# Kernel tuning notes

Hardware: AMD Instinct MI355X
Metric: run time of the kernel (lower is better)

The kernel has to match this reference:

```python
import jax, jax.numpy as jnp
import numpy as np

B, C, T, NB, NF = 4, 256, 128, 64, 512

def _rms(x, w, eps=1e-6):
    # RMSNorm over channel dim (axis=1) of NCHW tensor
    return x * jax.lax.rsqrt(jnp.mean(x * x, axis=1, keepdims=True) + eps) * w[None, :, None, None]

def _conv1(x, w, b):
    # 1x1 conv: w is [out, in]
    return jnp.einsum('bchw,oc->bohw', x, w) + b[None, :, None, None]

def _swiglu(x, iw, ib, ow, ob):
    h = _conv1(x, iw, ib)
    a, g = jnp.split(h, 2, axis=1)
    return _conv1(a * jax.nn.silu(g), ow, ob)

def setup_inputs() -> dict:
    key = jax.random.key(0)
    ks = iter(jax.random.split(key, 32))
    s = lambda shape, scale: jax.random.normal(next(ks), shape, jnp.float32) * scale
    wsc = 1.0 / np.sqrt(C)
    return {
        'latent': s((B, C, T, NB), 1.0),
        'side': s((B, C, T, NF), 1.0),
        'expansion_basis': s((1, NB, 1, NF), 1.0),
        'lp_norm_w': jnp.ones((C,), jnp.float32),
        'lp_w': s((C, C), wsc), 'lp_b': jnp.zeros((C,), jnp.float32),
        'qn_w': jnp.ones((C,), jnp.float32),
        'qmlp_in_w': s((2 * C, C), wsc), 'qmlp_in_b': jnp.zeros((2 * C,), jnp.float32),
        'qmlp_out_w': s((C, C), wsc), 'qmlp_out_b': jnp.zeros((C,), jnp.float32),
        'q_w': s((C, C), wsc), 'q_b': jnp.zeros((C,), jnp.float32),
        'k_w': s((C, C), wsc), 'k_b': jnp.zeros((C,), jnp.float32),
        'v_w': s((C, C), wsc), 'v_b': jnp.zeros((C,), jnp.float32),
        'o_w': s((C, C), wsc), 'o_b': jnp.zeros((C,), jnp.float32),
        'ffn_norm_w': jnp.ones((C,), jnp.float32),
        'ffn_in_w': s((2 * C, C), wsc), 'ffn_in_b': jnp.zeros((2 * C,), jnp.float32),
        'ffn_out_w': s((C, C), wsc), 'ffn_out_b': jnp.zeros((C,), jnp.float32),
        'score_scale': jnp.asarray(1.0 / np.sqrt(C), jnp.float32),
        'prior_scale': jnp.asarray(1.0, jnp.float32),
        'query_skip_scale': jnp.asarray(1.0, jnp.float32),
    }

def reference(latent, side, expansion_basis, lp_norm_w, lp_w, lp_b, qn_w,
              qmlp_in_w, qmlp_in_b, qmlp_out_w, qmlp_out_b,
              q_w, q_b, k_w, k_b, v_w, v_b, o_w, o_b,
              ffn_norm_w, ffn_in_w, ffn_in_b, ffn_out_w, ffn_out_b,
              score_scale, prior_scale, query_skip_scale):
    # latent_pre: RMSNorm -> 1x1 conv -> SiLU
    latent_h = jax.nn.silu(_conv1(_rms(latent, lp_norm_w), lp_w, lp_b))  # [B,C,T,NB]
    # adaptive query path
    query_h = _swiglu(_rms(side, qn_w), qmlp_in_w, qmlp_in_b, qmlp_out_w, qmlp_out_b)  # [B,C,T,NF]
    q = _conv1(query_h, q_w, q_b)   # [B,C,T,NF]
    k = _conv1(latent_h, k_w, k_b)  # [B,C,T,NB]
    v = _conv1(latent_h, v_w, v_b)  # [B,C,T,NB]
    # scores: [B,T,NF,NB], contraction over channel
    scores = jnp.einsum('bctf,bctn->btfn', q, k) * score_scale
    bias = expansion_basis[0, :, 0, :].T  # [NF, NB]
    scores = scores + bias[None, None] * prior_scale
    weights = jax.nn.softmax(scores, axis=-1)
    attended = jnp.einsum('btfn,bctn->bctf', weights, v)  # [B,C,T,NF]
    hidden = _conv1(attended, o_w, o_b) + query_h * query_skip_scale
    hidden = hidden + _swiglu(_rms(hidden, ffn_norm_w), ffn_in_w, ffn_in_b, ffn_out_w, ffn_out_b)
    return hidden
```

## Files before the change

kernel.cpp:

```cpp
#include <hip/hip_runtime.h>
#include <stdint.h>
#include <stddef.h>

#define B_ 4
#define C_ 256
#define T_ 128
#define NB_ 64
#define NF_ 512
#define PLAT_ (T_*NB_)
#define PSIDE_ (T_*NF_)

using bf16x8 = __attribute__((ext_vector_type(8))) short;
using bf16x4 = __attribute__((ext_vector_type(4))) short;
using f32x4  = __attribute__((ext_vector_type(4))) float;

__device__ __forceinline__ float b2f(unsigned short h) {
  unsigned int u = ((unsigned int)h) << 16;
  return __builtin_bit_cast(float, u);
}
__device__ __forceinline__ float b2f(short h) {
  unsigned int u = ((unsigned int)(unsigned short)h) << 16;
  return __builtin_bit_cast(float, u);
}
__device__ __forceinline__ unsigned short f2b(float f) {
  unsigned int u = __builtin_bit_cast(unsigned int, f);
  u += 0x7FFFu + ((u >> 16) & 1u);
  return (unsigned short)(u >> 16);
}

__device__ __forceinline__ bf16x8 ld8(const unsigned short* p) {
  return *(const bf16x8*)p;
}
__device__ __forceinline__ bf16x8 ld8(const float* p) {
  float4 a = *(const float4*)p;
  float4 b = *(const float4*)(p + 4);
  bf16x8 r;
  r[0] = (short)f2b(a.x); r[1] = (short)f2b(a.y);
  r[2] = (short)f2b(a.z); r[3] = (short)f2b(a.w);
  r[4] = (short)f2b(b.x); r[5] = (short)f2b(b.y);
  r[6] = (short)f2b(b.z); r[7] = (short)f2b(b.w);
  return r;
}
__device__ __forceinline__ void stv(float* p, float v) { *p = v; }
__device__ __forceinline__ void stv(unsigned short* p, float v) { *p = f2b(v); }

__device__ __forceinline__ void gload16(const void* g, void* l) {
  __builtin_amdgcn_global_load_lds(
      (const __attribute__((address_space(1))) void*)g,
      (__attribute__((address_space(3))) void*)l, 16, 0, 0);
}

__device__ __forceinline__ int u4i(int r) { return (r ^ (r >> 2)) & 3; }

enum { EPI_NONE = 0, EPI_SILU = 1, EPI_RESID = 3, EPI_SWIGLU = 4, EPI_DUALX = 5 };

__global__ __launch_bounds__(256) void wprep_k(const float* __restrict__ w,
                                               const float* __restrict__ nw,
                                               unsigned short* __restrict__ out, int n)
{
  int i = blockIdx.x * 256 + threadIdx.x;
  if (i < n) out[i] = f2b(w[i] * nw[i & 255]);
}

__global__ __launch_bounds__(256) void cvt_k(const float* __restrict__ in,
                                             unsigned short* __restrict__ out, int n)
{
  int i = blockIdx.x * 256 + threadIdx.x;
  if (i < n) out[i] = f2b(in[i]);
}

__global__ __launch_bounds__(256) void wscale_k(const float* __restrict__ w,
                                                const float* __restrict__ s,
                                                unsigned short* __restrict__ out, int n)
{
  int i = blockIdx.x * 256 + threadIdx.x;
  if (i < n) out[i] = f2b(w[i] * s[0]);
}

__global__ __launch_bounds__(256) void foldw_k(const float* __restrict__ A,
                                               const float* __restrict__ Bm,
                                               unsigned short* __restrict__ out)
{
  const int m = blockIdx.x;
  const int c = threadIdx.x;
  float acc = 0.f;
  #pragma unroll 8
  for (int j = 0; j < C_; ++j) acc = fmaf(A[m * C_ + j], Bm[j * C_ + c], acc);
  out[m * C_ + c] = f2b(acc);
}

__global__ __launch_bounds__(256) void foldb_k(const float* __restrict__ A,
                                               const float* __restrict__ bin,
                                               const float* __restrict__ badd,
                                               float* __restrict__ bout)
{
  const int m = threadIdx.x;
  float acc = 0.f;
  #pragma unroll 8
  for (int j = 0; j < C_; ++j) acc = fmaf(A[m * C_ + j], bin[j], acc);
  bout[m] = acc + badd[m];
}

__global__ __launch_bounds__(256) void bcomb_k(const float* __restrict__ b0,
                                               const float* __restrict__ b1,
                                               const float* __restrict__ s,
                                               float* __restrict__ bout)
{
  const int m = threadIdx.x;
  bout[m] = b0[m] + s[0] * b1[m];
}

template<int EPI, bool RMS, bool XT, typename TY, bool YT, int CFG, bool CSIN>
__global__ __launch_bounds__(256, 2) void gemm_k(
    const void* __restrict__ Xv,
    const void* __restrict__ Xv2,
    const unsigned short* __restrict__ W,
    const float* __restrict__ bias,
    TY* Y,
    const unsigned short* __restrict__ RT,
    float* pscale,
    int Xs, int Xoff, int Ys, int Yoff, int Ps)
{
  constexpr bool WDUAL = (EPI == EPI_SWIGLU) || (EPI == EPI_DUALX);
  constexpr bool GDUAL = (EPI == EPI_SWIGLU);
  constexpr bool XDUAL = (EPI == EPI_DUALX);
  constexpr int BM  = (CFG == 0) ? 256 : 128;
  constexpr int NWV = (CFG == 0) ? 1 : 2;
  constexpr int WN  = 64 / NWV;
  constexpr int NFR = WN / 16;
  constexpr int RW  = (WDUAL ? 2 : 1) * BM;
  constexpr int XR  = (XDUAL ? 2 : 1) * 64;

  __shared__ unsigned short sA[RW * 32];
  __shared__ unsigned short sX[XR * 32];
  __shared__ float red[4][64];

  const int tid = threadIdx.x;
  const int lane = tid & 63;
  const int wid = tid >> 6;
  const int l15 = lane & 15;
  const int q4 = lane >> 4;
  const int z = blockIdx.z;
  const int p0 = ((CFG == 0) ? blockIdx.x : (blockIdx.x >> 1)) * 64;
  const int m0 = (CFG == 0) ? 0 : (blockIdx.x & 1) * BM;
  const int mh = (CFG == 0) ? wid : (wid >> 1);
  const int nh = (CFG == 0) ? 0 : (wid & 1);

  const float* Xf = nullptr;
  const unsigned short* Xt = nullptr;
  const unsigned short* Xt2 = nullptr;
  if constexpr (XT) {
    Xt = (const unsigned short*)Xv + ((size_t)z * Xs + Xoff + p0) * C_;
    if constexpr (XDUAL)
      Xt2 = (const unsigned short*)Xv2 + ((size_t)z * Xs + Xoff + p0) * C_;
  } else {
    Xf = (const float*)Xv + (size_t)z * C_ * Xs + Xoff + p0;
  }

  const f32x4 zf = {0.f, 0.f, 0.f, 0.f};
  f32x4 acc0[4][NFR];
  f32x4 acc1[GDUAL ? 4 : 1][NFR];
  #pragma unroll
  for (int i = 0; i < 4; ++i)
    #pragma unroll
    for (int j = 0; j < NFR; ++j) {
      acc0[i][j] = zf;
      if constexpr (GDUAL) acc1[i][j] = zf;
    }

  float sq = 0.f;

  for (int kt = 0; kt < 8; ++kt) {
    if constexpr (XT) {
      const int row = wid * 16 + (lane >> 2);
      const int chunk = (lane & 3) ^ u4i(row);
      const size_t soff = (size_t)row * C_ + kt * 32 + (chunk << 3);
      gload16(Xt + soff, &sX[(wid * 16) * 32]);
      if constexpr (XDUAL) gload16(Xt2 + soff, &sX[(64 + wid * 16) * 32]);
    } else {
      const float* xp = Xf + (size_t)(kt * 32 + wid * 8) * Xs + lane;
      float v[8];
      #pragma unroll
      for (int j = 0; j < 8; ++j) v[j] = xp[(size_t)j * Xs];
      bf16x8 w8;
      #pragma unroll
      for (int j = 0; j < 8; ++j) {
        if constexpr (RMS) sq = fmaf(v[j], v[j], sq);
        w8[j] = (short)f2b(v[j]);
      }
      *(bf16x8*)((char*)sX + lane * 64 + ((wid ^ u4i(lane)) << 4)) = w8;
    }
    #pragma unroll
    for (int it = 0; it < RW / 64; ++it) {
      const int rbase = wid * (RW / 4) + it * 16;
      const int rl = rbase + (lane >> 2);
      const int bank = rl / BM;
      const int rloc = rl & (BM - 1);
      const int chunk = (lane & 3) ^ u4i(rl);
      gload16(W + (size_t)(bank * C_ + m0 + rloc) * C_ + kt * 32 + (chunk << 3),
              &sA[rbase * 32]);
    }
    __syncthreads();

    bf16x8 af0[4], af1[4], bfr[NFR], bfr2[NFR];
    #pragma unroll
    for (int mf = 0; mf < 4; ++mf) {
      const int r = mh * 64 + mf * 16 + l15;
      const int sl = (q4 ^ u4i(r)) << 3;
      af0[mf] = *(const bf16x8*)(&sA[r * 32 + sl]);
      if constexpr (WDUAL) af1[mf] = *(const bf16x8*)(&sA[(BM + r) * 32 + sl]);
    }
    #pragma unroll
    for (int nf = 0; nf < NFR; ++nf) {
      const int n = nh * WN + nf * 16 + l15;
      const int sl = (q4 ^ u4i(n)) << 3;
      bfr[nf] = *(const bf16x8*)(&sX[n * 32 + sl]);
      if constexpr (XDUAL) bfr2[nf] = *(const bf16x8*)(&sX[(64 + n) * 32 + sl]);
    }
    #pragma unroll
    for (int mf = 0; mf < 4; ++mf)
      #pragma unroll
      for (int nf = 0; nf < NFR; ++nf) {
        acc0[mf][nf] = __builtin_amdgcn_mfma_f32_16x16x32_bf16(af0[mf], bfr[nf], acc0[mf][nf], 0, 0, 0);
        if constexpr (GDUAL)
          acc1[mf][nf] = __builtin_amdgcn_mfma_f32_16x16x32_bf16(af1[mf], bfr[nf], acc1[mf][nf], 0, 0, 0);
        if constexpr (XDUAL)
          acc0[mf][nf] = __builtin_amdgcn_mfma_f32_16x16x32_bf16(af1[mf], bfr2[nf], acc0[mf][nf], 0, 0, 0);
      }
    __syncthreads();
  }

  float cs[NFR];
  #pragma unroll
  for (int nf = 0; nf < NFR; ++nf) cs[nf] = 1.f;
  if constexpr (RMS) {
    red[wid][lane] = sq;
    __syncthreads();
    #pragma unroll
    for (int nf = 0; nf < NFR; ++nf) {
      const int n = nh * WN + nf * 16 + l15;
      cs[nf] = rsqrtf((red[0][n] + red[1][n] + red[2][n] + red[3][n]) * (1.0f / (float)C_) + 1e-6f);
    }
  }
  if constexpr (CSIN) {
    #pragma unroll
    for (int nf = 0; nf < NFR; ++nf)
      cs[nf] = pscale[(size_t)z * Ps + p0 + nh * WN + nf * 16 + l15];
  }

  TY* Yb = nullptr;
  if constexpr (!YT) Yb = Y + (size_t)z * C_ * Ys + Yoff;

  float p2[NFR];
  #pragma unroll
  for (int nf = 0; nf < NFR; ++nf) p2[nf] = 0.f;

  #pragma unroll
  for (int mf = 0; mf < 4; ++mf) {
    const int mb = m0 + mh * 64 + mf * 16 + q4 * 4;
    const float4 b1 = *(const float4*)(bias + mb);
    float4 b2 = {0.f, 0.f, 0.f, 0.f};
    if constexpr (GDUAL) b2 = *(const float4*)(bias + C_ + mb);
    #pragma unroll
    for (int nf = 0; nf < NFR; ++nf) {
      const int pl = p0 + nh * WN + nf * 16 + l15;
      bf16x4 h4 = {0, 0, 0, 0};
      if constexpr (EPI == EPI_RESID)
        h4 = *(const bf16x4*)(RT + ((size_t)z * Ps + pl) * C_ + mb);
      if constexpr (YT) {
        bf16x4 pk;
        #pragma unroll
        for (int r = 0; r < 4; ++r) {
          float y = acc0[mf][nf][r] * cs[nf] + ((const float*)&b1)[r];
          if constexpr (EPI == EPI_SILU) y = y / (1.0f + __expf(-y));
          if constexpr (EPI == EPI_SWIGLU) {
            float g = acc1[mf][nf][r] * cs[nf] + ((const float*)&b2)[r];
            y = y * (g / (1.0f + __expf(-g)));
          }
          if constexpr (EPI == EPI_DUALX) p2[nf] = fmaf(y, y, p2[nf]);
          pk[r] = (short)f2b(y);
        }
        *(bf16x4*)(Y + ((size_t)z * Ys + Yoff + pl) * C_ + mb) = pk;
      } else {
        #pragma unroll
        for (int r = 0; r < 4; ++r) {
          const size_t oidx = (size_t)(mb + r) * Ys + pl;
          float y = acc0[mf][nf][r] * cs[nf] + ((const float*)&b1)[r];
          if constexpr (EPI == EPI_SILU) y = y / (1.0f + __expf(-y));
          if constexpr (EPI == EPI_SWIGLU) {
            float g = acc1[mf][nf][r] * cs[nf] + ((const float*)&b2)[r];
            y = y * (g / (1.0f + __expf(-g)));
          }
          if constexpr (EPI == EPI_RESID) y += b2f(h4[r]);
          stv(&Yb[oidx], y);
        }
      }
    }
  }

  if constexpr (EPI == EPI_DUALX) {
    #pragma unroll
    for (int nf = 0; nf < NFR; ++nf) {
      p2[nf] += __shfl_xor(p2[nf], 16);
      p2[nf] += __shfl_xor(p2[nf], 32);
    }
    if (q4 == 0) {
      #pragma unroll
      for (int nf = 0; nf < NFR; ++nf) red[wid][nf * 16 + l15] = p2[nf];
    }
    __syncthreads();
    if (wid == 0 && q4 == 0) {
      #pragma unroll
      for (int nf = 0; nf < NFR; ++nf) {
        const int n = nf * 16 + l15;
        const float c2 = rsqrtf((red[0][n] + red[1][n] + red[2][n] + red[3][n]) * (1.0f / (float)C_) + 1e-6f);
        pscale[(size_t)z * Ps + p0 + n] = c2;
      }
    }
  }
}

__global__ __launch_bounds__(256) void attn_k(
    const unsigned short* Q,
    const unsigned short* __restrict__ Kp,
    const unsigned short* __restrict__ Vp,
    const float* __restrict__ basis,
    const float* __restrict__ ssp,
    const float* __restrict__ psp,
    unsigned short* O,
    int PsQ, int t0, int ltc)
{
  __shared__ unsigned short sK[64 * 256];
  __shared__ unsigned short sQ[64 * 256];
  __shared__ unsigned short sV[256 * 72];
  __shared__ unsigned short sW[64 * 72];
  __shared__ unsigned short sB[64 * 72];

  const int tid = threadIdx.x;
  const int lane = tid & 63;
  const int wid = tid >> 6;
  const int l15 = lane & 15;
  const int q4 = lane >> 4;
  const int z = blockIdx.x >> ltc;
  const int tl = blockIdx.x & ((1 << ltc) - 1);

  const unsigned short* Qt = Q + ((size_t)z * PsQ + (size_t)tl * NF_) * C_;
  unsigned short*       Ot = O + ((size_t)z * PsQ + (size_t)tl * NF_) * C_;
  const unsigned short* Kt = Kp + ((size_t)z * PLAT_ + (size_t)(t0 + tl) * NB_) * C_;
  const size_t vbase = (size_t)z * C_ * PLAT_ + (size_t)(t0 + tl) * NB_;

  const float ss = ssp[0];
  const float ps = psp[0];
  const f32x4 zf = {0.f, 0.f, 0.f, 0.f};

  {
    #pragma unroll
    for (int it = 0; it < 8; ++it) {
      int i = wid * 8 + it;
      int n = 2 * i + (lane >> 5);
      int sc = (lane & 31) ^ (n & 7);
      gload16(Kt + (size_t)n * C_ + (sc << 3), &sK[i * 512]);
    }
    const int c0 = tid >> 3;
    const int n0 = (tid & 7) << 3;
    #pragma unroll
    for (int pass = 0; pass < 8; ++pass) {
      int c = c0 + pass * 32;
      bf16x8 v8 = *(const bf16x8*)(Vp + vbase + (size_t)c * PLAT_ + n0);
      *(bf16x8*)(&sV[c * 72 + n0]) = v8;
    }
  }

  for (int fc = 0; fc < 8; ++fc) {
    const int f0 = fc * 64;
    #pragma unroll
    for (int it = 0; it < 8; ++it) {
      int i = wid * 8 + it;
      int n = 2 * i + (lane >> 5);
      int sc = (lane & 31) ^ (n & 7);
      gload16(Qt + (size_t)(f0 + n) * C_ + (sc << 3), &sQ[i * 512]);
    }
    {
      const int nr = tid >> 3;
      const int fl0 = (tid & 7) << 3;
      #pragma unroll
      for (int pass = 0; pass < 2; ++pass) {
        int nn = nr + pass * 32;
        bf16x8 b8 = ld8(basis + (size_t)nn * NF_ + f0 + fl0);
        *(bf16x8*)(&sB[nn * 72 + fl0]) = b8;
      }
    }
    __syncthreads();

    f32x4 sacc[4];
    #pragma unroll
    for (int nt = 0; nt < 4; ++nt) sacc[nt] = zf;
    const int frow = wid * 16 + l15;
    const int swq = l15 & 7;
    #pragma unroll
    for (int kt = 0; kt < 8; ++kt) {
      int kb = kt * 4 + q4;
      bf16x8 a8 = *(const bf16x8*)(&sQ[frow * 256 + ((kb ^ swq) << 3)]);
      #pragma unroll
      for (int nt = 0; nt < 4; ++nt) {
        bf16x8 b8 = *(const bf16x8*)(&sK[(nt * 16 + l15) * 256 + ((kb ^ swq) << 3)]);
        sacc[nt] = __builtin_amdgcn_mfma_f32_16x16x32_bf16(a8, b8, sacc[nt], 0, 0, 0);
      }
    }

    #pragma unroll
    for (int r = 0; r < 4; ++r) {
      const int fcl = wid * 16 + q4 * 4 + r;
      float v[4];
      #pragma unroll
      for (int nt = 0; nt < 4; ++nt)
        v[nt] = sacc[nt][r] * ss + b2f(sB[(nt * 16 + l15) * 72 + fcl]) * ps;
      float mx = fmaxf(fmaxf(v[0], v[1]), fmaxf(v[2], v[3]));
      #pragma unroll
      for (int d = 1; d < 16; d <<= 1) mx = fmaxf(mx, __shfl_xor(mx, d));
      float e[4], sum = 0.f;
      #pragma unroll
      for (int nt = 0; nt < 4; ++nt) { e[nt] = __expf(v[nt] - mx); sum += e[nt]; }
      #pragma unroll
      for (int d = 1; d < 16; d <<= 1) sum += __shfl_xor(sum, d);
      float inv = 1.0f / sum;
      #pragma unroll
      for (int nt = 0; nt < 4; ++nt)
        sW[fcl * 72 + nt * 16 + l15] = f2b(e[nt] * inv);
    }
    __syncthreads();

    f32x4 pacc[4][4];
    #pragma unroll
    for (int mf = 0; mf < 4; ++mf)
      #pragma unroll
      for (int nf = 0; nf < 4; ++nf) pacc[mf][nf] = zf;
    #pragma unroll
    for (int kt = 0; kt < 2; ++kt) {
      int k0 = kt * 32 + q4 * 8;
      bf16x8 a8[4], b8[4];
      #pragma unroll
      for (int mf = 0; mf < 4; ++mf)
        a8[mf] = *(const bf16x8*)(&sV[(wid * 64 + mf * 16 + l15) * 72 + k0]);
      #pragma unroll
      for (int nf = 0; nf < 4; ++nf)
        b8[nf] = *(const bf16x8*)(&sW[(nf * 16 + l15) * 72 + k0]);
      #pragma unroll
      for (int mf = 0; mf < 4; ++mf)
        #pragma unroll
        for (int nf = 0; nf < 4; ++nf)
          pacc[mf][nf] = __builtin_amdgcn_mfma_f32_16x16x32_bf16(a8[mf], b8[nf], pacc[mf][nf], 0, 0, 0);
    }
    #pragma unroll
    for (int mf = 0; mf < 4; ++mf) {
      int cb = wid * 64 + mf * 16 + q4 * 4;
      #pragma unroll
      for (int nf = 0; nf < 4; ++nf) {
        int f = f0 + nf * 16 + l15;
        bf16x4 pk;
        #pragma unroll
        for (int r = 0; r < 4; ++r) pk[r] = (short)f2b(pacc[mf][nf][r]);
        *(bf16x4*)(Ot + (size_t)f * C_ + cb) = pk;
      }
    }
    __syncthreads();
  }
}

extern "C" void kernel_launch(void* const* d_in, const int* in_sizes, int n_in,
                              void* d_out, int out_size, void* d_ws, size_t ws_size,
                              hipStream_t stream)
{
  (void)in_sizes; (void)n_in; (void)out_size;
  const float* latent     = (const float*)d_in[0];
  const float* side       = (const float*)d_in[1];
  const float* basis      = (const float*)d_in[2];
  const float* lp_norm_w  = (const float*)d_in[3];
  const float* lp_w       = (const float*)d_in[4];
  const float* lp_b       = (const float*)d_in[5];
  const float* qn_w       = (const float*)d_in[6];
  const float* qmlp_in_w  = (const float*)d_in[7];
  const float* qmlp_in_b  = (const float*)d_in[8];
  const float* qmlp_out_w = (const float*)d_in[9];
  const float* qmlp_out_b = (const float*)d_in[10];
  const float* q_w        = (const float*)d_in[11];
  const float* q_b        = (const float*)d_in[12];
  const float* k_w        = (const float*)d_in[13];
  const float* k_b        = (const float*)d_in[14];
  const float* v_w        = (const float*)d_in[15];
  const float* v_b        = (const float*)d_in[16];
  const float* o_w        = (const float*)d_in[17];
  const float* o_b        = (const float*)d_in[18];
  const float* ffn_norm_w = (const float*)d_in[19];
  const float* ffn_in_w   = (const float*)d_in[20];
  const float* ffn_in_b   = (const float*)d_in[21];
  const float* ffn_out_w  = (const float*)d_in[22];
  const float* ffn_out_b  = (const float*)d_in[23];
  const float* sc_scale   = (const float*)d_in[24];
  const float* pr_scale   = (const float*)d_in[25];
  const float* qk_scale   = (const float*)d_in[26];
  float* out = (float*)d_out;

  auto align256 = [](size_t b) { return (b + 255) & ~(size_t)255; };
  const size_t fixed_bytes =
      5 * align256((size_t)C_ * C_ * 2) +
      3 * align256((size_t)2 * C_ * C_ * 2) +
      2 * align256((size_t)C_ * 4) +
      3 * align256((size_t)B_ * C_ * PLAT_ * 2);
  int nc = 16;
  for (int c = 1; c <= 16; c <<= 1) {
    size_t Pcb = (size_t)PSIDE_ / c;
    size_t need = fixed_bytes + 2 * align256((size_t)B_ * C_ * Pcb * 2)
                + align256((size_t)B_ * Pcb * 4);
    if (need <= ws_size) { nc = c; break; }
  }
  const int Pc  = PSIDE_ / nc;
  const int Tc  = T_ / nc;
  int ltc = 0; while ((1 << ltc) < Tc) ++ltc;

  char* ws = (char*)d_ws;
  size_t off = 0;
  auto carve = [&](size_t bytes) -> char* {
    char* p = ws + off;
    off += (bytes + 255) & ~(size_t)255;
    return p;
  };
  unsigned short* wlp      = (unsigned short*)carve((size_t)C_ * C_ * 2);
  unsigned short* wqin     = (unsigned short*)carve((size_t)2 * C_ * C_ * 2);
  unsigned short* wffin    = (unsigned short*)carve((size_t)2 * C_ * C_ * 2);
  unsigned short* wk       = (unsigned short*)carve((size_t)C_ * C_ * 2);
  unsigned short* wv       = (unsigned short*)carve((size_t)C_ * C_ * 2);
  unsigned short* wfo      = (unsigned short*)carve((size_t)C_ * C_ * 2);
  unsigned short* wqeff    = (unsigned short*)carve((size_t)C_ * C_ * 2);
  unsigned short* wocat    = (unsigned short*)carve((size_t)2 * C_ * C_ * 2);
  float*          beff     = (float*)carve((size_t)C_ * 4);
  float*          bcomb    = (float*)carve((size_t)C_ * 4);
  unsigned short* latent_h = (unsigned short*)carve((size_t)B_ * C_ * PLAT_ * 2);
  unsigned short* kbuf     = (unsigned short*)carve((size_t)B_ * C_ * PLAT_ * 2);
  unsigned short* vbuf     = (unsigned short*)carve((size_t)B_ * C_ * PLAT_ * 2);
  unsigned short* big0     = (unsigned short*)carve((size_t)B_ * C_ * Pc * 2);
  unsigned short* qbuf     = (unsigned short*)carve((size_t)B_ * C_ * Pc * 2);
  float*          pscale   = (float*)carve((size_t)B_ * Pc * 4);

  const dim3 blk(256);
  const dim3 gLatA(PLAT_ / 64, 1, B_);
  const dim3 gChA(Pc / 64, 1, B_);
  const dim3 gChB(Pc / 64 * 2, 1, B_);
  const int NW = C_ * C_;

  wprep_k<<<dim3(NW / 256), blk, 0, stream>>>(lp_w, lp_norm_w, wlp, NW);
  wprep_k<<<dim3(2 * NW / 256), blk, 0, stream>>>(qmlp_in_w, qn_w, wqin, 2 * NW);
  wprep_k<<<dim3(2 * NW / 256), blk, 0, stream>>>(ffn_in_w, ffn_norm_w, wffin, 2 * NW);
  cvt_k<<<dim3(NW / 256), blk, 0, stream>>>(k_w, wk, NW);
  cvt_k<<<dim3(NW / 256), blk, 0, stream>>>(v_w, wv, NW);
  cvt_k<<<dim3(NW / 256), blk, 0, stream>>>(ffn_out_w, wfo, NW);
  foldw_k<<<dim3(C_), blk, 0, stream>>>(q_w, qmlp_out_w, wqeff);
  foldb_k<<<dim3(1), blk, 0, stream>>>(q_w, qmlp_out_b, q_b, beff);
  cvt_k<<<dim3(NW / 256), blk, 0, stream>>>(o_w, wocat, NW);
  wscale_k<<<dim3(NW / 256), blk, 0, stream>>>(qmlp_out_w, qk_scale, wocat + (size_t)NW, NW);
  bcomb_k<<<dim3(1), blk, 0, stream>>>(o_b, qmlp_out_b, qk_scale, bcomb);

  gemm_k<EPI_SILU, true, false, unsigned short, true, 0, false><<<gLatA, blk, 0, stream>>>(
      latent, nullptr, wlp, lp_b, latent_h, nullptr, nullptr, PLAT_, 0, PLAT_, 0, 0);
  gemm_k<EPI_NONE, false, true, unsigned short, true, 0, false><<<gLatA, blk, 0, stream>>>(
      latent_h, nullptr, wk, k_b, kbuf, nullptr, nullptr, PLAT_, 0, PLAT_, 0, 0);
  gemm_k<EPI_NONE, false, true, unsigned short, false, 0, false><<<gLatA, blk, 0, stream>>>(
      latent_h, nullptr, wv, v_b, vbuf, nullptr, nullptr, PLAT_, 0, PLAT_, 0, 0);

  for (int ch = 0; ch < nc; ++ch) {
    const int co = ch * Pc;
    const int t0 = ch * Tc;
    gemm_k<EPI_SWIGLU, true, false, unsigned short, true, 1, false><<<gChB, blk, 0, stream>>>(
        side, nullptr, wqin, qmlp_in_b, big0, nullptr, nullptr, PSIDE_, co, Pc, 0, 0);
    gemm_k<EPI_NONE, false, true, unsigned short, true, 0, false><<<gChA, blk, 0, stream>>>(
        big0, nullptr, wqeff, beff, qbuf, nullptr, nullptr, Pc, 0, Pc, 0, 0);
    attn_k<<<dim3(B_ * Tc), blk, 0, stream>>>(qbuf, kbuf, vbuf, basis, sc_scale, pr_scale,
                                              qbuf, Pc, t0, ltc);
    gemm_k<EPI_DUALX, false, true, unsigned short, true, 0, false><<<gChA, blk, 0, stream>>>(
        qbuf, big0, wocat, bcomb, qbuf, nullptr, pscale, Pc, 0, Pc, 0, Pc);
    gemm_k<EPI_SWIGLU, false, true, unsigned short, true, 1, true><<<gChB, blk, 0, stream>>>(
        qbuf, nullptr, wffin, ffn_in_b, big0, nullptr, pscale, Pc, 0, Pc, 0, Pc);
    gemm_k<EPI_RESID, false, true, float, false, 0, false><<<gChA, blk, 0, stream>>>(
        big0, nullptr, wfo, ffn_out_b, out, qbuf, nullptr, Pc, 0, PSIDE_, co, Pc);
  }
}
```

Measured before the change: 1.285 ms.

## Pre-transpose side input to bf16 and widen GEMM N-tile to 128

```diff
diff --git a/kernel.cpp b/kernel.cpp
--- a/kernel.cpp
+++ b/kernel.cpp
@@ -110,7 +110,47 @@
   bout[m] = b0[m] + s[0] * b1[m];
 }
 
-template<int EPI, bool RMS, bool XT, typename TY, bool YT, int CFG, bool CSIN>
+__global__ __launch_bounds__(256) void xpose_k(
+    const float* __restrict__ X, unsigned short* __restrict__ XT,
+    float* __restrict__ PS, int Xs, int Xoff, int Pl)
+{
+  __shared__ unsigned short sT[64 * 256];
+  __shared__ float red[4][64];
+  const int tid = threadIdx.x;
+  const int lane = tid & 63;
+  const int wid = tid >> 6;
+  const int z = blockIdx.z;
+  const int p0 = blockIdx.x * 64;
+  const float* Xb = X + (size_t)z * C_ * Xs + Xoff + p0;
+
+  float sq = 0.f;
+  #pragma unroll
+  for (int kt = 0; kt < 8; ++kt) {
+    const float* xp = Xb + (size_t)(kt * 32 + wid * 8) * Xs + lane;
+    float v[8];
+    #pragma unroll
+    for (int j = 0; j < 8; ++j) v[j] = xp[(size_t)j * Xs];
+    bf16x8 w8;
+    #pragma unroll
+    for (int j = 0; j < 8; ++j) { sq = fmaf(v[j], v[j], sq); w8[j] = (short)f2b(v[j]); }
+    const int ch = kt * 4 + wid;
+    *(bf16x8*)(&sT[lane * 256 + ((ch ^ (lane & 31)) << 3)]) = w8;
+  }
+  red[wid][lane] = sq;
+  __syncthreads();
+  if (tid < 64)
+    PS[(size_t)z * Pl + p0 + tid] =
+        rsqrtf((red[0][tid] + red[1][tid] + red[2][tid] + red[3][tid]) * (1.0f / (float)C_) + 1e-6f);
+  #pragma unroll
+  for (int it = 0; it < 8; ++it) {
+    const int p = it * 8 + (tid >> 5);
+    const int ch = tid & 31;
+    bf16x8 val = *(const bf16x8*)(&sT[p * 256 + ((ch ^ (p & 31)) << 3)]);
+    *(bf16x8*)(&XT[((size_t)z * Pl + p0 + p) * C_ + ch * 8]) = val;
+  }
+}
+
+template<int EPI, bool RMS, bool XT, typename TY, bool YT, int CFG, bool CSIN, int BN>
 __global__ __launch_bounds__(256, 2) void gemm_k(
     const void* __restrict__ Xv,
     const void* __restrict__ Xv2,
@@ -126,14 +166,14 @@
   constexpr bool XDUAL = (EPI == EPI_DUALX);
   constexpr int BM  = (CFG == 0) ? 256 : 128;
   constexpr int NWV = (CFG == 0) ? 1 : 2;
-  constexpr int WN  = 64 / NWV;
+  constexpr int WN  = BN / NWV;
   constexpr int NFR = WN / 16;
   constexpr int RW  = (WDUAL ? 2 : 1) * BM;
-  constexpr int XR  = (XDUAL ? 2 : 1) * 64;
+  constexpr int XR  = (XDUAL ? 2 : 1) * BN;
 
   __shared__ unsigned short sA[RW * 32];
   __shared__ unsigned short sX[XR * 32];
-  __shared__ float red[4][64];
+  __shared__ float red[4][BN];
 
   const int tid = threadIdx.x;
   const int lane = tid & 63;
@@ -141,7 +181,7 @@
   const int l15 = lane & 15;
   const int q4 = lane >> 4;
   const int z = blockIdx.z;
-  const int p0 = ((CFG == 0) ? blockIdx.x : (blockIdx.x >> 1)) * 64;
+  const int p0 = ((CFG == 0) ? blockIdx.x : (blockIdx.x >> 1)) * BN;
   const int m0 = (CFG == 0) ? 0 : (blockIdx.x & 1) * BM;
   const int mh = (CFG == 0) ? wid : (wid >> 1);
   const int nh = (CFG == 0) ? 0 : (wid & 1);
@@ -159,7 +199,7 @@
 
   const f32x4 zf = {0.f, 0.f, 0.f, 0.f};
   f32x4 acc0[4][NFR];
-  f32x4 acc1[GDUAL ? 4 : 1][NFR];
+  f32x4 acc1[GDUAL ? 4 : 1][GDUAL ? NFR : 1];
   #pragma unroll
   for (int i = 0; i < 4; ++i)
     #pragma unroll
@@ -172,11 +212,15 @@
 
   for (int kt = 0; kt < 8; ++kt) {
     if constexpr (XT) {
-      const int row = wid * 16 + (lane >> 2);
-      const int chunk = (lane & 3) ^ u4i(row);
-      const size_t soff = (size_t)row * C_ + kt * 32 + (chunk << 3);
-      gload16(Xt + soff, &sX[(wid * 16) * 32]);
-      if constexpr (XDUAL) gload16(Xt2 + soff, &sX[(64 + wid * 16) * 32]);
+      #pragma unroll
+      for (int j2 = 0; j2 < BN / 64; ++j2) {
+        const int rbase = wid * (BN / 4) + j2 * 16;
+        const int row = rbase + (lane >> 2);
+        const int chunk = (lane & 3) ^ u4i(row);
+        const size_t soff = (size_t)row * C_ + kt * 32 + (chunk << 3);
+        gload16(Xt + soff, &sX[rbase * 32]);
+        if constexpr (XDUAL) gload16(Xt2 + soff, &sX[(BN + rbase) * 32]);
+      }
     } else {
       const float* xp = Xf + (size_t)(kt * 32 + wid * 8) * Xs + lane;
       float v[8];
@@ -215,7 +259,7 @@
       const int n = nh * WN + nf * 16 + l15;
       const int sl = (q4 ^ u4i(n)) << 3;
       bfr[nf] = *(const bf16x8*)(&sX[n * 32 + sl]);
-      if constexpr (XDUAL) bfr2[nf] = *(const bf16x8*)(&sX[(64 + n) * 32 + sl]);
+      if constexpr (XDUAL) bfr2[nf] = *(const bf16x8*)(&sX[(BN + n) * 32 + sl]);
     }
     #pragma unroll
     for (int mf = 0; mf < 4; ++mf)
@@ -510,8 +554,8 @@
   int nc = 16;
   for (int c = 1; c <= 16; c <<= 1) {
     size_t Pcb = (size_t)PSIDE_ / c;
-    size_t need = fixed_bytes + 2 * align256((size_t)B_ * C_ * Pcb * 2)
-                + align256((size_t)B_ * Pcb * 4);
+    size_t need = fixed_bytes + 3 * align256((size_t)B_ * C_ * Pcb * 2)
+                + 2 * align256((size_t)B_ * Pcb * 4);
     if (need <= ws_size) { nc = c; break; }
   }
   const int Pc  = PSIDE_ / nc;
@@ -540,12 +584,16 @@
   unsigned short* vbuf     = (unsigned short*)carve((size_t)B_ * C_ * PLAT_ * 2);
   unsigned short* big0     = (unsigned short*)carve((size_t)B_ * C_ * Pc * 2);
   unsigned short* qbuf     = (unsigned short*)carve((size_t)B_ * C_ * Pc * 2);
+  unsigned short* sideT    = (unsigned short*)carve((size_t)B_ * C_ * Pc * 2);
   float*          pscale   = (float*)carve((size_t)B_ * Pc * 4);
+  float*          spscale  = (float*)carve((size_t)B_ * Pc * 4);
 
   const dim3 blk(256);
-  const dim3 gLatA(PLAT_ / 64, 1, B_);
-  const dim3 gChA(Pc / 64, 1, B_);
-  const dim3 gChB(Pc / 64 * 2, 1, B_);
+  const dim3 gLat64(PLAT_ / 64, 1, B_);
+  const dim3 gLat128(PLAT_ / 128, 1, B_);
+  const dim3 gCh64(Pc / 64, 1, B_);
+  const dim3 gCh128(Pc / 128, 1, B_);
+  const dim3 gChB(Pc / 128 * 2, 1, B_);
   const int NW = C_ * C_;
 
   wprep_k<<<dim3(NW / 256), blk, 0, stream>>>(lp_w, lp_norm_w, wlp, NW);
@@ -560,27 +608,28 @@
   wscale_k<<<dim3(NW / 256), blk, 0, stream>>>(qmlp_out_w, qk_scale, wocat + (size_t)NW, NW);
   bcomb_k<<<dim3(1), blk, 0, stream>>>(o_b, qmlp_out_b, qk_scale, bcomb);
 
-  gemm_k<EPI_SILU, true, false, unsigned short, true, 0, false><<<gLatA, blk, 0, stream>>>(
+  gemm_k<EPI_SILU, true, false, unsigned short, true, 0, false, 64><<<gLat64, blk, 0, stream>>>(
       latent, nullptr, wlp, lp_b, latent_h, nullptr, nullptr, PLAT_, 0, PLAT_, 0, 0);
-  gemm_k<EPI_NONE, false, true, unsigned short, true, 0, false><<<gLatA, blk, 0, stream>>>(
+  gemm_k<EPI_NONE, false, true, unsigned short, true, 0, false, 128><<<gLat128, blk, 0, stream>>>(
       latent_h, nullptr, wk, k_b, kbuf, nullptr, nullptr, PLAT_, 0, PLAT_, 0, 0);
-  gemm_k<EPI_NONE, false, true, unsigned short, false, 0, false><<<gLatA, blk, 0, stream>>>(
+  gemm_k<EPI_NONE, false, true, unsigned short, false, 0, false, 128><<<gLat128, blk, 0, stream>>>(
       latent_h, nullptr, wv, v_b, vbuf, nullptr, nullptr, PLAT_, 0, PLAT_, 0, 0);
 
   for (int ch = 0; ch < nc; ++ch) {
     const int co = ch * Pc;
     const int t0 = ch * Tc;
-    gemm_k<EPI_SWIGLU, true, false, unsigned short, true, 1, false><<<gChB, blk, 0, stream>>>(
-        side, nullptr, wqin, qmlp_in_b, big0, nullptr, nullptr, PSIDE_, co, Pc, 0, 0);
-    gemm_k<EPI_NONE, false, true, unsigned short, true, 0, false><<<gChA, blk, 0, stream>>>(
+    xpose_k<<<gCh64, blk, 0, stream>>>(side, sideT, spscale, PSIDE_, co, Pc);
+    gemm_k<EPI_SWIGLU, false, true, unsigned short, true, 1, true, 128><<<gChB, blk, 0, stream>>>(
+        sideT, nullptr, wqin, qmlp_in_b, big0, nullptr, spscale, Pc, 0, Pc, 0, Pc);
+    gemm_k<EPI_NONE, false, true, unsigned short, true, 0, false, 128><<<gCh128, blk, 0, stream>>>(
         big0, nullptr, wqeff, beff, qbuf, nullptr, nullptr, Pc, 0, Pc, 0, 0);
     attn_k<<<dim3(B_ * Tc), blk, 0, stream>>>(qbuf, kbuf, vbuf, basis, sc_scale, pr_scale,
                                               qbuf, Pc, t0, ltc);
-    gemm_k<EPI_DUALX, false, true, unsigned short, true, 0, false><<<gChA, blk, 0, stream>>>(
+    gemm_k<EPI_DUALX, false, true, unsigned short, true, 0, false, 64><<<gCh64, blk, 0, stream>>>(
         qbuf, big0, wocat, bcomb, qbuf, nullptr, pscale, Pc, 0, Pc, 0, Pc);
-    gemm_k<EPI_SWIGLU, false, true, unsigned short, true, 1, true><<<gChB, blk, 0, stream>>>(
+    gemm_k<EPI_SWIGLU, false, true, unsigned short, true, 1, true, 128><<<gChB, blk, 0, stream>>>(
         qbuf, nullptr, wffin, ffn_in_b, big0, nullptr, pscale, Pc, 0, Pc, 0, Pc);
-    gemm_k<EPI_RESID, false, true, float, false, 0, false><<<gChA, blk, 0, stream>>>(
+    gemm_k<EPI_RESID, false, true, float, false, 0, false, 128><<<gCh128, blk, 0, stream>>>(
         big0, nullptr, wfo, ffn_out_b, out, qbuf, nullptr, Pc, 0, PSIDE_, co, Pc);
   }
 }
```

Measured after the change: 1.296 ms. Within noise of the previous version (+0.9%).
